# Optimization experiments

Measured on AMD Instinct MI355X. Metric: run time of the kernel, lower is better.

Reference implementation:

```python
import jax, jax.numpy as jnp
import numpy as np
import math

B, S, D, H, HD, FF, L, NS = 16, 512, 256, 8, 32, 1024, 2, 1024
THETA = 10000.0
EPS = 1e-5


def setup_inputs() -> dict:
    key = jax.random.key(0)
    ks = jax.random.split(key, 20)
    n = lambda i, shape: jax.random.normal(ks[i], shape, jnp.float32) * 0.02
    inp = {
        'values': jax.random.normal(ks[0], (B, S), jnp.float32),
        'dib': jax.random.uniform(ks[1], (B, S), jnp.float32),
        'gamma': jax.random.uniform(ks[2], (B, S), jnp.float32),
        'memory_type': jnp.ones((B, S), jnp.float32),
        'key_padding_mask': jnp.ones((B, S), dtype=bool),
        # input projection Linear(5, D)
        'in_w': n(3, (5, D)), 'in_b': jnp.zeros((D,), jnp.float32),
        # per-layer params stacked on leading L axis
        'ln1_s': jnp.ones((L, D), jnp.float32), 'ln1_b': jnp.zeros((L, D), jnp.float32),
        'qw': n(4, (L, D, D)), 'qb': jnp.zeros((L, D), jnp.float32),
        'kw': n(5, (L, D, D)), 'kb': jnp.zeros((L, D), jnp.float32),
        'vw': n(6, (L, D, D)), 'vb': jnp.zeros((L, D), jnp.float32),
        'ow': n(7, (L, D, D)), 'ob': jnp.zeros((L, D), jnp.float32),
        'ln2_s': jnp.ones((L, D), jnp.float32), 'ln2_b': jnp.zeros((L, D), jnp.float32),
        'ffw1': n(8, (L, D, FF)), 'ffb1': jnp.zeros((L, FF), jnp.float32),
        'ffw2': n(9, (L, FF, D)), 'ffb2': jnp.zeros((L, D), jnp.float32),
        'fn_s': jnp.ones((D,), jnp.float32), 'fn_b': jnp.zeros((D,), jnp.float32),
        # output head Linear(S*D, NS)
        'head_w': n(10, (S * D, NS)), 'head_b': jnp.zeros((NS,), jnp.float32),
    }
    return inp


def _layernorm(x, s, b):
    m = jnp.mean(x, axis=-1, keepdims=True)
    v = jnp.mean(jnp.square(x - m), axis=-1, keepdims=True)
    return (x - m) * jax.lax.rsqrt(v + EPS) * s + b


def _rotate_half(x):
    x1, x2 = jnp.split(x, 2, axis=-1)
    return jnp.concatenate((-x2, x1), axis=-1)


def _rope_tables():
    pos = jnp.arange(S, dtype=jnp.float32)
    inv_freq = 1.0 / (THETA ** (jnp.arange(0, HD, 2, dtype=jnp.float32) / HD))
    freqs = pos[:, None] * inv_freq[None, :]           # [S, HD/2]
    emb = jnp.concatenate((freqs, freqs), axis=-1)      # [S, HD]
    return jnp.cos(emb), jnp.sin(emb)


def _forward(values, dib, gamma, memory_type, key_padding_mask,
             in_w, in_b, ln1_s, ln1_b, qw, qb, kw, kb, vw, vb, ow, ob,
             ln2_s, ln2_b, ffw1, ffb1, ffw2, ffb2, fn_s, fn_b, head_w, head_b):
    # token features: (sign, magnitude, gamma, dib, memory_type in {-1,+1})
    sign = jnp.where(values >= 0, 1.0, -1.0)
    mt = memory_type * 2.0 - 1.0  # values in [0,1] -> signed encoding
    features = jnp.stack((sign, jnp.abs(values), gamma, dib, mt), axis=-1)  # [B,S,5]
    x = features @ in_w + in_b  # [B,S,D]

    cos, sin = _rope_tables()  # [S,HD]
    cos4 = cos[None, None]     # [1,1,S,HD]
    sin4 = sin[None, None]
    mask = key_padding_mask    # [B,S] bool
    neg = jnp.finfo(x.dtype).min
    scale = 1.0 / math.sqrt(HD)

    for l in range(L):
        h = _layernorm(x, ln1_s[l], ln1_b[l])
        q = (h @ qw[l] + qb[l]).reshape(B, S, H, HD).transpose(0, 2, 1, 3)  # [B,H,S,HD]
        k = (h @ kw[l] + kb[l]).reshape(B, S, H, HD).transpose(0, 2, 1, 3)
        v = (h @ vw[l] + vb[l]).reshape(B, S, H, HD).transpose(0, 2, 1, 3)
        q = q * cos4 + _rotate_half(q) * sin4
        k = k * cos4 + _rotate_half(k) * sin4
        scores = jnp.einsum('bhqd,bhkd->bhqk', q, k) * scale  # [B,H,S,S]
        scores = jnp.where(mask[:, None, None, :], scores, neg)
        attn = jax.nn.softmax(scores, axis=-1)
        ctx = jnp.einsum('bhqk,bhkd->bhqd', attn, v)
        ctx = ctx.transpose(0, 2, 1, 3).reshape(B, S, D)
        out = (ctx @ ow[l] + ob[l]) * mask[..., None].astype(x.dtype)
        x = x + out
        h2 = _layernorm(x, ln2_s[l], ln2_b[l])
        ff = jax.nn.gelu(h2 @ ffw1[l] + ffb1[l], approximate=False) @ ffw2[l] + ffb2[l]
        x = x + ff

    x = _layernorm(x, fn_s, fn_b)
    logits = x.reshape(B, S * D) @ head_w + head_b  # [B,NS]
    return logits


def reference(values, dib, gamma, memory_type, key_padding_mask,
              in_w, in_b, ln1_s, ln1_b, qw, qb, kw, kb, vw, vb, ow, ob,
              ln2_s, ln2_b, ffw1, ffb1, ffw2, ffb2, fn_s, fn_b, head_w, head_b):
    return _forward(values, dib, gamma, memory_type, key_padding_mask,
                    in_w, in_b, ln1_s, ln1_b, qw, qb, kw, kb, vw, vb, ow, ob,
                    ln2_s, ln2_b, ffw1, ffb1, ffw2, ffb2, fn_s, fn_b, head_w, head_b)
```

## Files before the change

kernel.cpp:

```cpp
#include <hip/hip_runtime.h>
#include <math.h>

#define BB 16
#define SS 512
#define DD 256
#define HH 8
#define HDIM 32
#define FFD 1024
#define NL 2
#define NSOUT 1024
#define SD (SS*DD)
#define ROWS (BB*SS)

#define HEAD_KC 256
#define HEAD_NCH 512

typedef __attribute__((ext_vector_type(8))) short short8;
typedef __attribute__((ext_vector_type(4))) float f32x4;

__device__ __forceinline__ unsigned short f2bf(float f) {
    union { float f; unsigned u; } c; c.f = f;
    unsigned u = c.u + 0x7fffu + ((c.u >> 16) & 1u);
    return (unsigned short)(u >> 16);
}

__device__ __forceinline__ float wave_sum(float v) {
#pragma unroll
    for (int off = 32; off > 0; off >>= 1) v += __shfl_xor(v, off);
    return v;
}
__device__ __forceinline__ float wave_max(float v) {
#pragma unroll
    for (int off = 32; off > 0; off >>= 1) v = fmaxf(v, __shfl_xor(v, off));
    return v;
}

__global__ __launch_bounds__(256) void k_rope_table(float* ct, float* st) {
    int i = blockIdx.x * 256 + threadIdx.x;
    if (i >= SS * 16) return;
    int s = i >> 4, f = i & 15;
    float invf = powf(10000.f, -(float)f / 16.f);
    float ang = (float)s * invf;
    ct[i] = cosf(ang);
    st[i] = sinf(ang);
}

__global__ __launch_bounds__(256) void k_prep_t(
    const float* __restrict__ src, unsigned short* __restrict__ dst, int K, int N) {
    __shared__ float tile[32][33];
    size_t zo = (size_t)blockIdx.z * K * N;
    int k0 = blockIdx.x * 32, n0 = blockIdx.y * 32;
    int t = threadIdx.x;
    int r = t >> 3, c4 = (t & 7) * 4;
    float4 a = *(const float4*)&src[zo + (size_t)(k0 + r) * N + n0 + c4];
    tile[r][c4 + 0] = a.x; tile[r][c4 + 1] = a.y; tile[r][c4 + 2] = a.z; tile[r][c4 + 3] = a.w;
    __syncthreads();
    unsigned o0 = f2bf(tile[c4 + 0][r]), o1 = f2bf(tile[c4 + 1][r]);
    unsigned o2 = f2bf(tile[c4 + 2][r]), o3 = f2bf(tile[c4 + 3][r]);
    uint2 ud = { o0 | (o1 << 16), o2 | (o3 << 16) };
    *(uint2*)&dst[zo + (size_t)(n0 + r) * K + k0 + c4] = ud;
}

__global__ __launch_bounds__(256) void k_input_proj(
    const float* __restrict__ values, const float* __restrict__ dib,
    const float* __restrict__ gamma, const float* __restrict__ mtyp,
    const float* __restrict__ in_w, const float* __restrict__ in_b,
    float* __restrict__ x) {
    int i = blockIdx.x * 256 + threadIdx.x;
    int row = i >> 8, d = i & 255;
    float v = values[row];
    float f0 = (v >= 0.f) ? 1.f : -1.f;
    float f1 = fabsf(v);
    float f2 = gamma[row];
    float f3 = dib[row];
    float f4 = mtyp[row] * 2.f - 1.f;
    x[i] = f0 * in_w[d] + f1 * in_w[DD + d] + f2 * in_w[2 * DD + d]
         + f3 * in_w[3 * DD + d] + f4 * in_w[4 * DD + d] + in_b[d];
}

template <bool OBF>
__global__ __launch_bounds__(256) void k_layernorm(
    const float* __restrict__ in, void* __restrict__ outp,
    const float* __restrict__ sc, const float* __restrict__ bi) {
    int row = blockIdx.x;
    int t = threadIdx.x;
    float v = in[(size_t)row * DD + t];
    __shared__ float red[8];
    int wid = t >> 6, lane = t & 63;
    float s = wave_sum(v);
    if (lane == 0) red[wid] = s;
    __syncthreads();
    float mean = (red[0] + red[1] + red[2] + red[3]) * (1.f / DD);
    float dv = v - mean;
    float s2 = wave_sum(dv * dv);
    if (lane == 0) red[4 + wid] = s2;
    __syncthreads();
    float var = (red[4] + red[5] + red[6] + red[7]) * (1.f / DD);
    float o = dv * rsqrtf(var + 1e-5f) * sc[t] + bi[t];
    if (OBF) ((unsigned short*)outp)[(size_t)row * DD + t] = f2bf(o);
    else     ((float*)outp)[(size_t)row * DD + t] = o;
}

template <int EPI, bool OBF>
__global__ __launch_bounds__(256) void k_gemm_bf16(
    const short* __restrict__ A, const short* __restrict__ Bt,
    const float* __restrict__ bias, void* __restrict__ Cout,
    int M, int N, int K, const float* __restrict__ resx, const int* __restrict__ mask) {
    __shared__ __align__(16) short As[128 * 32];
    __shared__ __align__(16) short Bs[128 * 32];
    int t = threadIdx.x;
    int lane = t & 63, wid = t >> 6;
    int wr = wid >> 1, wc = wid & 1;
    int m0 = blockIdx.x * 128, n0 = blockIdx.y * 128;
    f32x4 acc[4][4] = {};
    int srow = t >> 2, sslot = t & 3;
    for (int k0 = 0; k0 < K; k0 += 32) {
#pragma unroll
        for (int p = 0; p < 2; ++p) {
            int row = srow + p * 64;
            int sw = sslot ^ ((row >> 1) & 3);
            *(float4*)&As[row * 32 + sw * 8] =
                *(const float4*)&A[(size_t)(m0 + row) * K + k0 + sslot * 8];
            *(float4*)&Bs[row * 32 + sw * 8] =
                *(const float4*)&Bt[(size_t)(n0 + row) * K + k0 + sslot * 8];
        }
        __syncthreads();
        short8 af[4], bfr[4];
#pragma unroll
        for (int mt = 0; mt < 4; ++mt) {
            int row = wr * 64 + mt * 16 + (lane & 15);
            int sl = (lane >> 4) ^ ((row >> 1) & 3);
            af[mt] = *(const short8*)&As[row * 32 + sl * 8];
        }
#pragma unroll
        for (int nt = 0; nt < 4; ++nt) {
            int row = wc * 64 + nt * 16 + (lane & 15);
            int sl = (lane >> 4) ^ ((row >> 1) & 3);
            bfr[nt] = *(const short8*)&Bs[row * 32 + sl * 8];
        }
#pragma unroll
        for (int mt = 0; mt < 4; ++mt)
#pragma unroll
            for (int nt = 0; nt < 4; ++nt)
                acc[mt][nt] = __builtin_amdgcn_mfma_f32_16x16x32_bf16(af[mt], bfr[nt], acc[mt][nt], 0, 0, 0);
        __syncthreads();
    }
#pragma unroll
    for (int mt = 0; mt < 4; ++mt) {
#pragma unroll
        for (int i = 0; i < 4; ++i) {
            int gm = m0 + wr * 64 + mt * 16 + (lane >> 4) * 4 + i;
            float mk = 1.f;
            if (EPI == 2) mk = (mask[gm] != 0) ? 1.f : 0.f;
#pragma unroll
            for (int nt = 0; nt < 4; ++nt) {
                int gn = n0 + wc * 64 + nt * 16 + (lane & 15);
                float v = acc[mt][nt][i] + bias[gn];
                if (EPI == 1) v = 0.5f * v * (1.f + erff(v * 0.70710678118654752f));
                if (EPI == 2 || EPI == 3) v = resx[(size_t)gm * N + gn] + v * mk;
                if (OBF) ((unsigned short*)Cout)[(size_t)gm * N + gn] = f2bf(v);
                else     ((float*)Cout)[(size_t)gm * N + gn] = v;
            }
        }
    }
}

template <int EPI>
__global__ __launch_bounds__(256) void k_gemm64(
    const short* __restrict__ A, const short* __restrict__ Bt,
    const float* __restrict__ bias, float* __restrict__ Cout,
    int M, int N, int K, const float* __restrict__ resx, const int* __restrict__ mask) {
    __shared__ __align__(16) short As[64 * 32];
    __shared__ __align__(16) short Bs[128 * 32];
    int t = threadIdx.x;
    int lane = t & 63, wid = t >> 6;
    int wr = wid >> 1, wc = wid & 1;
    int m0 = blockIdx.x * 64, n0 = blockIdx.y * 128;
    f32x4 acc[2][4] = {};
    int srow = t >> 2, sslot = t & 3;
    int l15 = lane & 15, lh = lane >> 4;
    for (int k0 = 0; k0 < K; k0 += 32) {
        {
            int sw = sslot ^ ((srow >> 1) & 3);
            *(float4*)&As[srow * 32 + sw * 8] =
                *(const float4*)&A[(size_t)(m0 + srow) * K + k0 + sslot * 8];
        }
#pragma unroll
        for (int p = 0; p < 2; ++p) {
            int row = srow + p * 64;
            int sw = sslot ^ ((row >> 1) & 3);
            *(float4*)&Bs[row * 32 + sw * 8] =
                *(const float4*)&Bt[(size_t)(n0 + row) * K + k0 + sslot * 8];
        }
        __syncthreads();
        short8 af[2], bfr[4];
#pragma unroll
        for (int mt = 0; mt < 2; ++mt) {
            int row = wr * 32 + mt * 16 + l15;
            int sl = lh ^ ((row >> 1) & 3);
            af[mt] = *(const short8*)&As[row * 32 + sl * 8];
        }
#pragma unroll
        for (int nt = 0; nt < 4; ++nt) {
            int row = wc * 64 + nt * 16 + l15;
            int sl = lh ^ ((row >> 1) & 3);
            bfr[nt] = *(const short8*)&Bs[row * 32 + sl * 8];
        }
#pragma unroll
        for (int mt = 0; mt < 2; ++mt)
#pragma unroll
            for (int nt = 0; nt < 4; ++nt)
                acc[mt][nt] = __builtin_amdgcn_mfma_f32_16x16x32_bf16(af[mt], bfr[nt], acc[mt][nt], 0, 0, 0);
        __syncthreads();
    }
#pragma unroll
    for (int mt = 0; mt < 2; ++mt) {
#pragma unroll
        for (int i = 0; i < 4; ++i) {
            int gm = m0 + wr * 32 + mt * 16 + lh * 4 + i;
            float mk = 1.f;
            if (EPI == 2) mk = (mask[gm] != 0) ? 1.f : 0.f;
#pragma unroll
            for (int nt = 0; nt < 4; ++nt) {
                int gn = n0 + wc * 64 + nt * 16 + l15;
                float v = acc[mt][nt][i] + bias[gn];
                v = resx[(size_t)gm * N + gn] + v * mk;
                Cout[(size_t)gm * N + gn] = v;
            }
        }
    }
}

__global__ __launch_bounds__(256) void k_qkv(
    const short* __restrict__ A,
    const short* __restrict__ Wq, const short* __restrict__ Wk, const short* __restrict__ Wv,
    const float* __restrict__ bq, const float* __restrict__ bk, const float* __restrict__ bv,
    const float* __restrict__ ct, const float* __restrict__ st,
    unsigned short* __restrict__ q16, unsigned short* __restrict__ k16,
    unsigned short* __restrict__ vt16) {
    __shared__ __align__(16) short As[128 * 32];
    __shared__ __align__(16) short Bs[128 * 32];
    int mat = blockIdx.y >> 1;
    int n0 = (blockIdx.y & 1) * 128;
    const short* Bt = (mat == 0) ? Wq : (mat == 1) ? Wk : Wv;
    const float* bias = (mat == 0) ? bq : (mat == 1) ? bk : bv;
    int t = threadIdx.x;
    int lane = t & 63, wid = t >> 6;
    int wr = wid >> 1, wc = wid & 1;
    int m0 = blockIdx.x * 128;
    int l15 = lane & 15, lh = lane >> 4;
    f32x4 acc[4][4] = {};
    int srow = t >> 2, sslot = t & 3;
    for (int k0 = 0; k0 < DD; k0 += 32) {
#pragma unroll
        for (int p = 0; p < 2; ++p) {
            int row = srow + p * 64;
            int sw = sslot ^ ((row >> 1) & 3);
            *(float4*)&As[row * 32 + sw * 8] =
                *(const float4*)&A[(size_t)(m0 + row) * DD + k0 + sslot * 8];
            *(float4*)&Bs[row * 32 + sw * 8] =
                *(const float4*)&Bt[(size_t)(n0 + row) * DD + k0 + sslot * 8];
        }
        __syncthreads();
        short8 af[4], bfr[4];
#pragma unroll
        for (int mt = 0; mt < 4; ++mt) {
            int row = wr * 64 + mt * 16 + l15;
            int sl = lh ^ ((row >> 1) & 3);
            af[mt] = *(const short8*)&As[row * 32 + sl * 8];
        }
#pragma unroll
        for (int nt = 0; nt < 4; ++nt) {
            int row = wc * 64 + nt * 16 + l15;
            int sl = lh ^ ((row >> 1) & 3);
            bfr[nt] = *(const short8*)&Bs[row * 32 + sl * 8];
        }
#pragma unroll
        for (int mt = 0; mt < 4; ++mt)
#pragma unroll
            for (int nt = 0; nt < 4; ++nt)
                acc[mt][nt] = __builtin_amdgcn_mfma_f32_16x16x32_bf16(af[mt], bfr[nt], acc[mt][nt], 0, 0, 0);
        __syncthreads();
    }
    float bs[4];
#pragma unroll
    for (int nt = 0; nt < 4; ++nt) bs[nt] = bias[n0 + wc * 64 + nt * 16 + l15];
    if (mat < 2) {
        unsigned short* dst = (mat == 0) ? q16 : k16;
#pragma unroll
        for (int mt = 0; mt < 4; ++mt) {
#pragma unroll
            for (int i = 0; i < 4; ++i) {
                int gm = m0 + wr * 64 + mt * 16 + lh * 4 + i;
                int s = gm & (SS - 1);
                float c = ct[s * 16 + l15], sn = st[s * 16 + l15];
                float val[4];
#pragma unroll
                for (int nt = 0; nt < 4; ++nt) val[nt] = acc[mt][nt][i] + bs[nt];
#pragma unroll
                for (int nt = 0; nt < 4; ++nt) {
                    float partner = val[nt ^ 1];
                    float o = ((nt & 1) == 0) ? (val[nt] * c - partner * sn)
                                              : (val[nt] * c + partner * sn);
                    dst[(size_t)gm * DD + n0 + wc * 64 + nt * 16 + l15] = f2bf(o);
                }
            }
        }
    } else {
#pragma unroll
        for (int mt = 0; mt < 4; ++mt) {
            int gmb = m0 + wr * 64 + mt * 16 + lh * 4;
            int b = gmb >> 9, sb = gmb & (SS - 1);
#pragma unroll
            for (int nt = 0; nt < 4; ++nt) {
                int gn = n0 + wc * 64 + nt * 16 + l15;
                int h = gn >> 5, d = gn & 31;
                ushort4 u;
#pragma unroll
                for (int i = 0; i < 4; ++i)
                    (&u.x)[i] = f2bf(acc[mt][nt][i] + bs[nt]);
                *(ushort4*)&vt16[((size_t)((b * HH + h) * HDIM + d)) * SS + sb] = u;
            }
        }
    }
}

__global__ __launch_bounds__(256) void k_flash(
    const short* __restrict__ qb, const short* __restrict__ kb,
    const short* __restrict__ vt, const int* __restrict__ mask,
    unsigned short* __restrict__ ctxb) {
    __shared__ float bias_lds[SS];
    __shared__ __align__(16) short p_lds[4][32 * 72];
    __shared__ __align__(16) float r_lds[4][32];
    int t = threadIdx.x, lane = t & 63, wq = t >> 6;
    int bh = blockIdx.y;
    int b = bh >> 3, h = bh & 7;
    int q0 = blockIdx.x * 128 + wq * 32;
    bias_lds[t]       = (mask[b * SS + t]       != 0) ? 0.f : -3.0e38f;
    bias_lds[t + 256] = (mask[b * SS + t + 256] != 0) ? 0.f : -3.0e38f;
    __syncthreads();
    int l15 = lane & 15, lh = lane >> 4;
    short8 qfr[2];
    qfr[0] = *(const short8*)&qb[((size_t)(b * SS) + q0 + l15) * DD + h * HDIM + lh * 8];
    qfr[1] = *(const short8*)&qb[((size_t)(b * SS) + q0 + 16 + l15) * DD + h * HDIM + lh * 8];
    float m[2] = {-3.0e38f, -3.0e38f};
    float lsum[2] = {0.f, 0.f};
    f32x4 oacc[2][2] = {};
    const float scale = 0.17677669529663687f;
    for (int k0 = 0; k0 < SS; k0 += 64) {
        f32x4 sT[4][2];
#pragma unroll
        for (int kt = 0; kt < 4; ++kt) {
            short8 kf = *(const short8*)&kb[((size_t)(b * SS) + k0 + kt * 16 + l15) * DD + h * HDIM + lh * 8];
#pragma unroll
            for (int qf = 0; qf < 2; ++qf) {
                f32x4 z = {0.f, 0.f, 0.f, 0.f};
                sT[kt][qf] = __builtin_amdgcn_mfma_f32_16x16x32_bf16(kf, qfr[qf], z, 0, 0, 0);
            }
        }
        float p[2][16];
        float r[2];
#pragma unroll
        for (int qf = 0; qf < 2; ++qf) {
            float pmax = -3.0e38f;
#pragma unroll
            for (int kt = 0; kt < 4; ++kt)
#pragma unroll
                for (int i = 0; i < 4; ++i) {
                    float s = sT[kt][qf][i] * scale + bias_lds[k0 + kt * 16 + lh * 4 + i];
                    p[qf][kt * 4 + i] = s;
                    pmax = fmaxf(pmax, s);
                }
            pmax = fmaxf(pmax, __shfl_xor(pmax, 16));
            pmax = fmaxf(pmax, __shfl_xor(pmax, 32));
            float mn = fmaxf(m[qf], pmax);
            r[qf] = expf(m[qf] - mn);
            m[qf] = mn;
            float cs = 0.f;
#pragma unroll
            for (int j = 0; j < 16; ++j) {
                float e = expf(p[qf][j] - mn);
                p[qf][j] = e;
                cs += e;
            }
            cs += __shfl_xor(cs, 16);
            cs += __shfl_xor(cs, 32);
            lsum[qf] = lsum[qf] * r[qf] + cs;
        }
#pragma unroll
        for (int qf = 0; qf < 2; ++qf) {
            int qq = qf * 16 + l15;
#pragma unroll
            for (int kt = 0; kt < 4; ++kt) {
                unsigned u0 = (unsigned)f2bf(p[qf][kt * 4 + 0]) | ((unsigned)f2bf(p[qf][kt * 4 + 1]) << 16);
                unsigned u1 = (unsigned)f2bf(p[qf][kt * 4 + 2]) | ((unsigned)f2bf(p[qf][kt * 4 + 3]) << 16);
                uint2 u = { u0, u1 };
                *(uint2*)&p_lds[wq][qq * 72 + kt * 16 + lh * 4] = u;
            }
        }
        if (lane < 16) { r_lds[wq][l15] = r[0]; r_lds[wq][16 + l15] = r[1]; }
        __syncthreads();
#pragma unroll
        for (int mf = 0; mf < 2; ++mf) {
            float4 rv = *(const float4*)&r_lds[wq][mf * 16 + lh * 4];
#pragma unroll
            for (int df = 0; df < 2; ++df) {
                oacc[mf][df][0] *= rv.x; oacc[mf][df][1] *= rv.y;
                oacc[mf][df][2] *= rv.z; oacc[mf][df][3] *= rv.w;
            }
        }
#pragma unroll
        for (int ks = 0; ks < 2; ++ks) {
            short8 pa0 = *(const short8*)&p_lds[wq][(l15) * 72 + ks * 32 + lh * 8];
            short8 pa1 = *(const short8*)&p_lds[wq][(16 + l15) * 72 + ks * 32 + lh * 8];
#pragma unroll
            for (int df = 0; df < 2; ++df) {
                short8 vf = *(const short8*)&vt[((size_t)bh * HDIM + df * 16 + l15) * SS + k0 + ks * 32 + lh * 8];
                oacc[0][df] = __builtin_amdgcn_mfma_f32_16x16x32_bf16(pa0, vf, oacc[0][df], 0, 0, 0);
                oacc[1][df] = __builtin_amdgcn_mfma_f32_16x16x32_bf16(pa1, vf, oacc[1][df], 0, 0, 0);
            }
        }
        __syncthreads();
    }
    if (lane < 16) { r_lds[wq][l15] = 1.f / lsum[0]; r_lds[wq][16 + l15] = 1.f / lsum[1]; }
    __syncthreads();
#pragma unroll
    for (int mf = 0; mf < 2; ++mf) {
        float4 lv = *(const float4*)&r_lds[wq][mf * 16 + lh * 4];
        const float li[4] = { lv.x, lv.y, lv.z, lv.w };
#pragma unroll
        for (int df = 0; df < 2; ++df)
#pragma unroll
            for (int i = 0; i < 4; ++i) {
                int gq = q0 + mf * 16 + lh * 4 + i;
                int gd = df * 16 + l15;
                ctxb[((size_t)(b * SS) + gq) * DD + h * HDIM + gd] = f2bf(oacc[mf][df][i] * li[i]);
            }
    }
}

__global__ __launch_bounds__(256) void k_head_part(
    const float* __restrict__ x, const float* __restrict__ W,
    float* __restrict__ part) {
    __shared__ float xs[16 * HEAD_KC];
    int c = blockIdx.x;
    int k0 = c * HEAD_KC;
    int t = threadIdx.x;
#pragma unroll
    for (int b = 0; b < 16; ++b)
        xs[b * HEAD_KC + t] = x[(size_t)b * SD + k0 + t];
    __syncthreads();
    int n4 = t * 4;
    float acc[16][4] = {};
#pragma unroll 4
    for (int k = 0; k < HEAD_KC; ++k) {
        float4 w = *(const float4*)&W[(size_t)(k0 + k) * NSOUT + n4];
#pragma unroll
        for (int b = 0; b < 16; ++b) {
            float xv = xs[b * HEAD_KC + k];
            acc[b][0] += xv * w.x; acc[b][1] += xv * w.y;
            acc[b][2] += xv * w.z; acc[b][3] += xv * w.w;
        }
    }
#pragma unroll
    for (int b = 0; b < 16; ++b) {
        float4 o = {acc[b][0], acc[b][1], acc[b][2], acc[b][3]};
        *(float4*)&part[((size_t)c * 16 + b) * NSOUT + n4] = o;
    }
}

__global__ __launch_bounds__(256) void k_head_reduce(
    const float* __restrict__ part, const float* __restrict__ hb,
    float* __restrict__ out) {
    int i = (blockIdx.x * 256 + threadIdx.x) * 4;
    float4 s = {0.f, 0.f, 0.f, 0.f};
#pragma unroll 8
    for (int c = 0; c < HEAD_NCH; ++c) {
        float4 p = *(const float4*)&part[(size_t)c * (16 * NSOUT) + i];
        s.x += p.x; s.y += p.y; s.z += p.z; s.w += p.w;
    }
    int n = i & (NSOUT - 1);
    float4 b4 = *(const float4*)&hb[n];
    float4 o = {s.x + b4.x, s.y + b4.y, s.z + b4.z, s.w + b4.w};
    *(float4*)&out[i] = o;
}

extern "C" void kernel_launch(void* const* d_in, const int* in_sizes, int n_in,
                              void* d_out, int out_size, void* d_ws, size_t ws_size,
                              hipStream_t stream) {
    const float* values = (const float*)d_in[0];
    const float* dib    = (const float*)d_in[1];
    const float* gamma  = (const float*)d_in[2];
    const float* mtyp   = (const float*)d_in[3];
    const int*   mask   = (const int*)d_in[4];
    const float* in_w   = (const float*)d_in[5];
    const float* in_b   = (const float*)d_in[6];
    const float* ln1_s  = (const float*)d_in[7];
    const float* ln1_b  = (const float*)d_in[8];
    const float* p_qw   = (const float*)d_in[9];
    const float* p_qb   = (const float*)d_in[10];
    const float* p_kw   = (const float*)d_in[11];
    const float* p_kb   = (const float*)d_in[12];
    const float* p_vw   = (const float*)d_in[13];
    const float* p_vb   = (const float*)d_in[14];
    const float* p_ow   = (const float*)d_in[15];
    const float* p_ob   = (const float*)d_in[16];
    const float* ln2_s  = (const float*)d_in[17];
    const float* ln2_b  = (const float*)d_in[18];
    const float* p_f1w  = (const float*)d_in[19];
    const float* p_f1b  = (const float*)d_in[20];
    const float* p_f2w  = (const float*)d_in[21];
    const float* p_f2b  = (const float*)d_in[22];
    const float* fn_s   = (const float*)d_in[23];
    const float* fn_b   = (const float*)d_in[24];
    const float* head_w = (const float*)d_in[25];
    const float* head_b = (const float*)d_in[26];
    float* out = (float*)d_out;

    const size_t MB = 1u << 20;
    char* w = (char*)d_ws;
    float* x    = (float*)(w + 0 * MB);
    float* qf   = (float*)(w + 8 * MB);
    unsigned short* h16  = (unsigned short*)(w + 32 * MB);
    unsigned short* q16  = (unsigned short*)(w + 36 * MB);
    unsigned short* k16  = (unsigned short*)(w + 40 * MB);
    unsigned short* vt16 = (unsigned short*)(w + 44 * MB);
    unsigned short* cx16 = (unsigned short*)(w + 48 * MB);
    unsigned short* f116 = (unsigned short*)(w + 52 * MB);
    unsigned short* wq16 = (unsigned short*)(w + 68 * MB);
    unsigned short* wk16 = (unsigned short*)(w + 68 * MB + 256 * 1024);
    unsigned short* wv16 = (unsigned short*)(w + 68 * MB + 512 * 1024);
    unsigned short* wo16 = (unsigned short*)(w + 68 * MB + 768 * 1024);
    unsigned short* wf116 = (unsigned short*)(w + 69 * MB);
    unsigned short* wf216 = (unsigned short*)(w + 70 * MB);
    float* ct   = (float*)(w + 71 * MB);
    float* st   = (float*)(w + 71 * MB + 64 * 1024);
    float* sc   = (float*)(w + 72 * MB);

    k_rope_table<<<32, 256, 0, stream>>>(ct, st);
    k_prep_t<<<dim3(8, 8, NL), 256, 0, stream>>>(p_qw, wq16, DD, DD);
    k_prep_t<<<dim3(8, 8, NL), 256, 0, stream>>>(p_kw, wk16, DD, DD);
    k_prep_t<<<dim3(8, 8, NL), 256, 0, stream>>>(p_vw, wv16, DD, DD);
    k_prep_t<<<dim3(8, 8, NL), 256, 0, stream>>>(p_ow, wo16, DD, DD);
    k_prep_t<<<dim3(8, 32, NL), 256, 0, stream>>>(p_f1w, wf116, DD, FFD);
    k_prep_t<<<dim3(32, 8, NL), 256, 0, stream>>>(p_f2w, wf216, FFD, DD);
    k_input_proj<<<8192, 256, 0, stream>>>(values, dib, gamma, mtyp, in_w, in_b, x);

    for (int l = 0; l < NL; ++l) {
        k_layernorm<true><<<ROWS, 256, 0, stream>>>(x, h16, ln1_s + l * DD, ln1_b + l * DD);
        k_qkv<<<dim3(64, 6), 256, 0, stream>>>((const short*)h16,
            (const short*)(wq16 + l * 65536), (const short*)(wk16 + l * 65536),
            (const short*)(wv16 + l * 65536),
            p_qb + l * DD, p_kb + l * DD, p_vb + l * DD, ct, st, q16, k16, vt16);
        k_flash<<<dim3(4, BB * HH), 256, 0, stream>>>((const short*)q16, (const short*)k16,
            (const short*)vt16, mask, cx16);
        k_gemm64<2><<<dim3(128, 2), 256, 0, stream>>>((const short*)cx16,
            (const short*)(wo16 + l * 65536), p_ob + l * DD, x, ROWS, DD, DD, x, mask);
        k_layernorm<true><<<ROWS, 256, 0, stream>>>(x, h16, ln2_s + l * DD, ln2_b + l * DD);
        k_gemm_bf16<1, true><<<dim3(64, 8), 256, 0, stream>>>((const short*)h16,
            (const short*)(wf116 + l * 262144), p_f1b + l * FFD, f116,
            ROWS, FFD, DD, nullptr, nullptr);
        k_gemm64<3><<<dim3(128, 2), 256, 0, stream>>>((const short*)f116,
            (const short*)(wf216 + l * 262144), p_f2b + l * DD, x, ROWS, DD, FFD, x, nullptr);
    }

    k_layernorm<false><<<ROWS, 256, 0, stream>>>(x, qf, fn_s, fn_b);
    k_head_part<<<HEAD_NCH, 256, 0, stream>>>(qf, head_w, sc);
    k_head_reduce<<<16, 256, 0, stream>>>(sc, head_b, out);
}
```

Baseline: 371.1 us.

## Merge prep kernels, wave-per-row layernorm, retile GEMMs, fold attention scale into Q

Merges the weight-transpose and RoPE-table kernels into a single launch, cutting launch overhead. Layernorm now gives each row to one wavefront with float4 loads and a one-pass sum and sum-of-squares, which removes block barriers. The k_gemm64 k-step grows to 64 with an 8-way swizzle, and QKV moves to 64-row tiles to launch more blocks. The softmax scale is folded into Q, attention uses fast __expf, and the head GEMM uses nontemporal weight loads with deeper unrolling. The one-pass variance and fast exp carry small numerical risk.

```diff
diff --git a/kernel.cpp b/kernel.cpp
--- a/kernel.cpp
+++ b/kernel.cpp
@@ -24,41 +24,52 @@
     return (unsigned short)(u >> 16);
 }
 
-__device__ __forceinline__ float wave_sum(float v) {
-#pragma unroll
-    for (int off = 32; off > 0; off >>= 1) v += __shfl_xor(v, off);
-    return v;
-}
-__device__ __forceinline__ float wave_max(float v) {
-#pragma unroll
-    for (int off = 32; off > 0; off >>= 1) v = fmaxf(v, __shfl_xor(v, off));
-    return v;
-}
-
-__global__ __launch_bounds__(256) void k_rope_table(float* ct, float* st) {
-    int i = blockIdx.x * 256 + threadIdx.x;
-    if (i >= SS * 16) return;
-    int s = i >> 4, f = i & 15;
-    float invf = powf(10000.f, -(float)f / 16.f);
-    float ang = (float)s * invf;
-    ct[i] = cosf(ang);
-    st[i] = sinf(ang);
-}
-
-__global__ __launch_bounds__(256) void k_prep_t(
-    const float* __restrict__ src, unsigned short* __restrict__ dst, int K, int N) {
+__global__ __launch_bounds__(256) void k_prep_all(
+    const float* __restrict__ p_qw, const float* __restrict__ p_kw,
+    const float* __restrict__ p_vw, const float* __restrict__ p_ow,
+    const float* __restrict__ p_f1w, const float* __restrict__ p_f2w,
+    unsigned short* __restrict__ wq, unsigned short* __restrict__ wk,
+    unsigned short* __restrict__ wv, unsigned short* __restrict__ wo,
+    unsigned short* __restrict__ wf1, unsigned short* __restrict__ wf2,
+    float* __restrict__ ct, float* __restrict__ st) {
+    int bid = blockIdx.x;
+    int t = threadIdx.x;
+    if (bid >= 1536) {
+        int i = (bid - 1536) * 256 + t;
+        if (i < SS * 16) {
+            int s = i >> 4, f = i & 15;
+            float invf = powf(10000.f, -(float)f / 16.f);
+            float ang = (float)s * invf;
+            ct[i] = cosf(ang);
+            st[i] = sinf(ang);
+        }
+        return;
+    }
+    const float* src; unsigned short* dst;
+    int K, N, kx, nx, l;
+    if (bid < 512) {
+        int grp = bid >> 7, r = bid & 127; l = r >> 6; int tl = r & 63;
+        kx = tl >> 3; nx = tl & 7; K = DD; N = DD;
+        src = grp == 0 ? p_qw : grp == 1 ? p_kw : grp == 2 ? p_vw : p_ow;
+        dst = grp == 0 ? wq : grp == 1 ? wk : grp == 2 ? wv : wo;
+    } else if (bid < 1024) {
+        int r = bid - 512; l = r >> 8; int tl = r & 255;
+        kx = tl >> 5; nx = tl & 31; K = DD; N = FFD; src = p_f1w; dst = wf1;
+    } else {
+        int r = bid - 1024; l = r >> 8; int tl = r & 255;
+        kx = tl >> 3; nx = tl & 7; K = FFD; N = DD; src = p_f2w; dst = wf2;
+    }
     __shared__ float tile[32][33];
-    size_t zo = (size_t)blockIdx.z * K * N;
-    int k0 = blockIdx.x * 32, n0 = blockIdx.y * 32;
-    int t = threadIdx.x;
-    int r = t >> 3, c4 = (t & 7) * 4;
-    float4 a = *(const float4*)&src[zo + (size_t)(k0 + r) * N + n0 + c4];
-    tile[r][c4 + 0] = a.x; tile[r][c4 + 1] = a.y; tile[r][c4 + 2] = a.z; tile[r][c4 + 3] = a.w;
+    size_t zo = (size_t)l * K * N;
+    int k0 = kx * 32, n0 = nx * 32;
+    int r_ = t >> 3, c4 = (t & 7) * 4;
+    float4 a = *(const float4*)&src[zo + (size_t)(k0 + r_) * N + n0 + c4];
+    tile[r_][c4 + 0] = a.x; tile[r_][c4 + 1] = a.y; tile[r_][c4 + 2] = a.z; tile[r_][c4 + 3] = a.w;
     __syncthreads();
-    unsigned o0 = f2bf(tile[c4 + 0][r]), o1 = f2bf(tile[c4 + 1][r]);
-    unsigned o2 = f2bf(tile[c4 + 2][r]), o3 = f2bf(tile[c4 + 3][r]);
+    unsigned o0 = f2bf(tile[c4 + 0][r_]), o1 = f2bf(tile[c4 + 1][r_]);
+    unsigned o2 = f2bf(tile[c4 + 2][r_]), o3 = f2bf(tile[c4 + 3][r_]);
     uint2 ud = { o0 | (o1 << 16), o2 | (o3 << 16) };
-    *(uint2*)&dst[zo + (size_t)(n0 + r) * K + k0 + c4] = ud;
+    *(uint2*)&dst[zo + (size_t)(n0 + r_) * K + k0 + c4] = ud;
 }
 
 __global__ __launch_bounds__(256) void k_input_proj(
@@ -79,33 +90,41 @@
 }
 
 template <bool OBF>
-__global__ __launch_bounds__(256) void k_layernorm(
+__global__ __launch_bounds__(256) void k_layernorm_w(
     const float* __restrict__ in, void* __restrict__ outp,
     const float* __restrict__ sc, const float* __restrict__ bi) {
-    int row = blockIdx.x;
-    int t = threadIdx.x;
-    float v = in[(size_t)row * DD + t];
-    __shared__ float red[8];
-    int wid = t >> 6, lane = t & 63;
-    float s = wave_sum(v);
-    if (lane == 0) red[wid] = s;
-    __syncthreads();
-    float mean = (red[0] + red[1] + red[2] + red[3]) * (1.f / DD);
-    float dv = v - mean;
-    float s2 = wave_sum(dv * dv);
-    if (lane == 0) red[4 + wid] = s2;
-    __syncthreads();
-    float var = (red[4] + red[5] + red[6] + red[7]) * (1.f / DD);
-    float o = dv * rsqrtf(var + 1e-5f) * sc[t] + bi[t];
-    if (OBF) ((unsigned short*)outp)[(size_t)row * DD + t] = f2bf(o);
-    else     ((float*)outp)[(size_t)row * DD + t] = o;
-}
-
-template <int EPI, bool OBF>
-__global__ __launch_bounds__(256) void k_gemm_bf16(
+    int t = threadIdx.x, lane = t & 63, w = t >> 6;
+    int row = blockIdx.x * 4 + w;
+    float4 v = *(const float4*)&in[(size_t)row * DD + lane * 4];
+    float s1 = v.x + v.y + v.z + v.w;
+    float s2 = v.x * v.x + v.y * v.y + v.z * v.z + v.w * v.w;
+#pragma unroll
+    for (int off = 32; off > 0; off >>= 1) {
+        s1 += __shfl_xor(s1, off);
+        s2 += __shfl_xor(s2, off);
+    }
+    float mean = s1 * (1.f / DD);
+    float var = s2 * (1.f / DD) - mean * mean;
+    float rstd = rsqrtf(var + 1e-5f);
+    float4 sv = *(const float4*)&sc[lane * 4];
+    float4 bv = *(const float4*)&bi[lane * 4];
+    float o0 = (v.x - mean) * rstd * sv.x + bv.x;
+    float o1 = (v.y - mean) * rstd * sv.y + bv.y;
+    float o2 = (v.z - mean) * rstd * sv.z + bv.z;
+    float o3 = (v.w - mean) * rstd * sv.w + bv.w;
+    if (OBF) {
+        ushort4 u = { f2bf(o0), f2bf(o1), f2bf(o2), f2bf(o3) };
+        *(ushort4*)&((unsigned short*)outp)[(size_t)row * DD + lane * 4] = u;
+    } else {
+        float4 o = { o0, o1, o2, o3 };
+        *(float4*)&((float*)outp)[(size_t)row * DD + lane * 4] = o;
+    }
+}
+
+__global__ __launch_bounds__(256) void k_gemm_ff1(
     const short* __restrict__ A, const short* __restrict__ Bt,
-    const float* __restrict__ bias, void* __restrict__ Cout,
-    int M, int N, int K, const float* __restrict__ resx, const int* __restrict__ mask) {
+    const float* __restrict__ bias, unsigned short* __restrict__ Cout,
+    int M, int N, int K) {
     __shared__ __align__(16) short As[128 * 32];
     __shared__ __align__(16) short Bs[128 * 32];
     int t = threadIdx.x;
@@ -150,16 +169,12 @@
 #pragma unroll
         for (int i = 0; i < 4; ++i) {
             int gm = m0 + wr * 64 + mt * 16 + (lane >> 4) * 4 + i;
-            float mk = 1.f;
-            if (EPI == 2) mk = (mask[gm] != 0) ? 1.f : 0.f;
 #pragma unroll
             for (int nt = 0; nt < 4; ++nt) {
                 int gn = n0 + wc * 64 + nt * 16 + (lane & 15);
                 float v = acc[mt][nt][i] + bias[gn];
-                if (EPI == 1) v = 0.5f * v * (1.f + erff(v * 0.70710678118654752f));
-                if (EPI == 2 || EPI == 3) v = resx[(size_t)gm * N + gn] + v * mk;
-                if (OBF) ((unsigned short*)Cout)[(size_t)gm * N + gn] = f2bf(v);
-                else     ((float*)Cout)[(size_t)gm * N + gn] = v;
+                v = 0.5f * v * (1.f + erff(v * 0.70710678118654752f));
+                Cout[(size_t)gm * N + gn] = f2bf(v);
             }
         }
     }
@@ -170,47 +185,53 @@
     const short* __restrict__ A, const short* __restrict__ Bt,
     const float* __restrict__ bias, float* __restrict__ Cout,
     int M, int N, int K, const float* __restrict__ resx, const int* __restrict__ mask) {
-    __shared__ __align__(16) short As[64 * 32];
-    __shared__ __align__(16) short Bs[128 * 32];
+    __shared__ __align__(16) short As[64 * 64];
+    __shared__ __align__(16) short Bs[128 * 64];
     int t = threadIdx.x;
     int lane = t & 63, wid = t >> 6;
     int wr = wid >> 1, wc = wid & 1;
     int m0 = blockIdx.x * 64, n0 = blockIdx.y * 128;
+    int l15 = lane & 15, lh = lane >> 4;
     f32x4 acc[2][4] = {};
-    int srow = t >> 2, sslot = t & 3;
-    int l15 = lane & 15, lh = lane >> 4;
-    for (int k0 = 0; k0 < K; k0 += 32) {
-        {
-            int sw = sslot ^ ((srow >> 1) & 3);
-            *(float4*)&As[srow * 32 + sw * 8] =
-                *(const float4*)&A[(size_t)(m0 + srow) * K + k0 + sslot * 8];
-        }
+    for (int k0 = 0; k0 < K; k0 += 64) {
 #pragma unroll
         for (int p = 0; p < 2; ++p) {
-            int row = srow + p * 64;
-            int sw = sslot ^ ((row >> 1) & 3);
-            *(float4*)&Bs[row * 32 + sw * 8] =
-                *(const float4*)&Bt[(size_t)(n0 + row) * K + k0 + sslot * 8];
-        }
-        __syncthreads();
-        short8 af[2], bfr[4];
-#pragma unroll
-        for (int mt = 0; mt < 2; ++mt) {
-            int row = wr * 32 + mt * 16 + l15;
-            int sl = lh ^ ((row >> 1) & 3);
-            af[mt] = *(const short8*)&As[row * 32 + sl * 8];
-        }
-#pragma unroll
-        for (int nt = 0; nt < 4; ++nt) {
-            int row = wc * 64 + nt * 16 + l15;
-            int sl = lh ^ ((row >> 1) & 3);
-            bfr[nt] = *(const short8*)&Bs[row * 32 + sl * 8];
-        }
-#pragma unroll
-        for (int mt = 0; mt < 2; ++mt)
-#pragma unroll
-            for (int nt = 0; nt < 4; ++nt)
-                acc[mt][nt] = __builtin_amdgcn_mfma_f32_16x16x32_bf16(af[mt], bfr[nt], acc[mt][nt], 0, 0, 0);
+            int idx = t + p * 256;
+            int row = idx >> 3, sl = idx & 7;
+            int sw = sl ^ (row & 7);
+            *(float4*)&As[row * 64 + sw * 8] =
+                *(const float4*)&A[(size_t)(m0 + row) * K + k0 + sl * 8];
+        }
+#pragma unroll
+        for (int p = 0; p < 4; ++p) {
+            int idx = t + p * 256;
+            int row = idx >> 3, sl = idx & 7;
+            int sw = sl ^ (row & 7);
+            *(float4*)&Bs[row * 64 + sw * 8] =
+                *(const float4*)&Bt[(size_t)(n0 + row) * K + k0 + sl * 8];
+        }
+        __syncthreads();
+#pragma unroll
+        for (int kk = 0; kk < 2; ++kk) {
+            short8 af[2], bfr[4];
+#pragma unroll
+            for (int mt = 0; mt < 2; ++mt) {
+                int row = wr * 32 + mt * 16 + l15;
+                int sl = (kk * 4 + lh) ^ (row & 7);
+                af[mt] = *(const short8*)&As[row * 64 + sl * 8];
+            }
+#pragma unroll
+            for (int nt = 0; nt < 4; ++nt) {
+                int row = wc * 64 + nt * 16 + l15;
+                int sl = (kk * 4 + lh) ^ (row & 7);
+                bfr[nt] = *(const short8*)&Bs[row * 64 + sl * 8];
+            }
+#pragma unroll
+            for (int mt = 0; mt < 2; ++mt)
+#pragma unroll
+                for (int nt = 0; nt < 4; ++nt)
+                    acc[mt][nt] = __builtin_amdgcn_mfma_f32_16x16x32_bf16(af[mt], bfr[nt], acc[mt][nt], 0, 0, 0);
+        }
         __syncthreads();
     }
 #pragma unroll
@@ -231,14 +252,14 @@
     }
 }
 
-__global__ __launch_bounds__(256) void k_qkv(
+__global__ __launch_bounds__(256) void k_qkv64(
     const short* __restrict__ A,
     const short* __restrict__ Wq, const short* __restrict__ Wk, const short* __restrict__ Wv,
     const float* __restrict__ bq, const float* __restrict__ bk, const float* __restrict__ bv,
     const float* __restrict__ ct, const float* __restrict__ st,
     unsigned short* __restrict__ q16, unsigned short* __restrict__ k16,
     unsigned short* __restrict__ vt16) {
-    __shared__ __align__(16) short As[128 * 32];
+    __shared__ __align__(16) short As[64 * 32];
     __shared__ __align__(16) short Bs[128 * 32];
     int mat = blockIdx.y >> 1;
     int n0 = (blockIdx.y & 1) * 128;
@@ -247,25 +268,28 @@
     int t = threadIdx.x;
     int lane = t & 63, wid = t >> 6;
     int wr = wid >> 1, wc = wid & 1;
-    int m0 = blockIdx.x * 128;
+    int m0 = blockIdx.x * 64;
     int l15 = lane & 15, lh = lane >> 4;
-    f32x4 acc[4][4] = {};
+    f32x4 acc[2][4] = {};
     int srow = t >> 2, sslot = t & 3;
     for (int k0 = 0; k0 < DD; k0 += 32) {
+        {
+            int sw = sslot ^ ((srow >> 1) & 3);
+            *(float4*)&As[srow * 32 + sw * 8] =
+                *(const float4*)&A[(size_t)(m0 + srow) * DD + k0 + sslot * 8];
+        }
 #pragma unroll
         for (int p = 0; p < 2; ++p) {
             int row = srow + p * 64;
             int sw = sslot ^ ((row >> 1) & 3);
-            *(float4*)&As[row * 32 + sw * 8] =
-                *(const float4*)&A[(size_t)(m0 + row) * DD + k0 + sslot * 8];
             *(float4*)&Bs[row * 32 + sw * 8] =
                 *(const float4*)&Bt[(size_t)(n0 + row) * DD + k0 + sslot * 8];
         }
         __syncthreads();
-        short8 af[4], bfr[4];
-#pragma unroll
-        for (int mt = 0; mt < 4; ++mt) {
-            int row = wr * 64 + mt * 16 + l15;
+        short8 af[2], bfr[4];
+#pragma unroll
+        for (int mt = 0; mt < 2; ++mt) {
+            int row = wr * 32 + mt * 16 + l15;
             int sl = lh ^ ((row >> 1) & 3);
             af[mt] = *(const short8*)&As[row * 32 + sl * 8];
         }
@@ -276,7 +300,7 @@
             bfr[nt] = *(const short8*)&Bs[row * 32 + sl * 8];
         }
 #pragma unroll
-        for (int mt = 0; mt < 4; ++mt)
+        for (int mt = 0; mt < 2; ++mt)
 #pragma unroll
             for (int nt = 0; nt < 4; ++nt)
                 acc[mt][nt] = __builtin_amdgcn_mfma_f32_16x16x32_bf16(af[mt], bfr[nt], acc[mt][nt], 0, 0, 0);
@@ -287,16 +311,17 @@
     for (int nt = 0; nt < 4; ++nt) bs[nt] = bias[n0 + wc * 64 + nt * 16 + l15];
     if (mat < 2) {
         unsigned short* dst = (mat == 0) ? q16 : k16;
-#pragma unroll
-        for (int mt = 0; mt < 4; ++mt) {
+        const float qscale = (mat == 0) ? 0.17677669529663687f : 1.f;
+#pragma unroll
+        for (int mt = 0; mt < 2; ++mt) {
 #pragma unroll
             for (int i = 0; i < 4; ++i) {
-                int gm = m0 + wr * 64 + mt * 16 + lh * 4 + i;
+                int gm = m0 + wr * 32 + mt * 16 + lh * 4 + i;
                 int s = gm & (SS - 1);
                 float c = ct[s * 16 + l15], sn = st[s * 16 + l15];
                 float val[4];
 #pragma unroll
-                for (int nt = 0; nt < 4; ++nt) val[nt] = acc[mt][nt][i] + bs[nt];
+                for (int nt = 0; nt < 4; ++nt) val[nt] = (acc[mt][nt][i] + bs[nt]) * qscale;
 #pragma unroll
                 for (int nt = 0; nt < 4; ++nt) {
                     float partner = val[nt ^ 1];
@@ -308,8 +333,8 @@
         }
     } else {
 #pragma unroll
-        for (int mt = 0; mt < 4; ++mt) {
-            int gmb = m0 + wr * 64 + mt * 16 + lh * 4;
+        for (int mt = 0; mt < 2; ++mt) {
+            int gmb = m0 + wr * 32 + mt * 16 + lh * 4;
             int b = gmb >> 9, sb = gmb & (SS - 1);
 #pragma unroll
             for (int nt = 0; nt < 4; ++nt) {
@@ -346,7 +371,6 @@
     float m[2] = {-3.0e38f, -3.0e38f};
     float lsum[2] = {0.f, 0.f};
     f32x4 oacc[2][2] = {};
-    const float scale = 0.17677669529663687f;
     for (int k0 = 0; k0 < SS; k0 += 64) {
         f32x4 sT[4][2];
 #pragma unroll
@@ -367,19 +391,19 @@
             for (int kt = 0; kt < 4; ++kt)
 #pragma unroll
                 for (int i = 0; i < 4; ++i) {
-                    float s = sT[kt][qf][i] * scale + bias_lds[k0 + kt * 16 + lh * 4 + i];
+                    float s = sT[kt][qf][i] + bias_lds[k0 + kt * 16 + lh * 4 + i];
                     p[qf][kt * 4 + i] = s;
                     pmax = fmaxf(pmax, s);
                 }
             pmax = fmaxf(pmax, __shfl_xor(pmax, 16));
             pmax = fmaxf(pmax, __shfl_xor(pmax, 32));
             float mn = fmaxf(m[qf], pmax);
-            r[qf] = expf(m[qf] - mn);
+            r[qf] = __expf(m[qf] - mn);
             m[qf] = mn;
             float cs = 0.f;
 #pragma unroll
             for (int j = 0; j < 16; ++j) {
-                float e = expf(p[qf][j] - mn);
+                float e = __expf(p[qf][j] - mn);
                 p[qf][j] = e;
                 cs += e;
             }
@@ -452,14 +476,14 @@
     __syncthreads();
     int n4 = t * 4;
     float acc[16][4] = {};
-#pragma unroll 4
+#pragma unroll 8
     for (int k = 0; k < HEAD_KC; ++k) {
-        float4 w = *(const float4*)&W[(size_t)(k0 + k) * NSOUT + n4];
+        f32x4 w = __builtin_nontemporal_load((const f32x4*)&W[(size_t)(k0 + k) * NSOUT + n4]);
 #pragma unroll
         for (int b = 0; b < 16; ++b) {
             float xv = xs[b * HEAD_KC + k];
-            acc[b][0] += xv * w.x; acc[b][1] += xv * w.y;
-            acc[b][2] += xv * w.z; acc[b][3] += xv * w.w;
+            acc[b][0] += xv * w[0]; acc[b][1] += xv * w[1];
+            acc[b][2] += xv * w[2]; acc[b][3] += xv * w[3];
         }
     }
 #pragma unroll
@@ -537,18 +561,13 @@
     float* st   = (float*)(w + 71 * MB + 64 * 1024);
     float* sc   = (float*)(w + 72 * MB);
 
-    k_rope_table<<<32, 256, 0, stream>>>(ct, st);
-    k_prep_t<<<dim3(8, 8, NL), 256, 0, stream>>>(p_qw, wq16, DD, DD);
-    k_prep_t<<<dim3(8, 8, NL), 256, 0, stream>>>(p_kw, wk16, DD, DD);
-    k_prep_t<<<dim3(8, 8, NL), 256, 0, stream>>>(p_vw, wv16, DD, DD);
-    k_prep_t<<<dim3(8, 8, NL), 256, 0, stream>>>(p_ow, wo16, DD, DD);
-    k_prep_t<<<dim3(8, 32, NL), 256, 0, stream>>>(p_f1w, wf116, DD, FFD);
-    k_prep_t<<<dim3(32, 8, NL), 256, 0, stream>>>(p_f2w, wf216, FFD, DD);
+    k_prep_all<<<1568, 256, 0, stream>>>(p_qw, p_kw, p_vw, p_ow, p_f1w, p_f2w,
+                                         wq16, wk16, wv16, wo16, wf116, wf216, ct, st);
     k_input_proj<<<8192, 256, 0, stream>>>(values, dib, gamma, mtyp, in_w, in_b, x);
 
     for (int l = 0; l < NL; ++l) {
-        k_layernorm<true><<<ROWS, 256, 0, stream>>>(x, h16, ln1_s + l * DD, ln1_b + l * DD);
-        k_qkv<<<dim3(64, 6), 256, 0, stream>>>((const short*)h16,
+        k_layernorm_w<true><<<2048, 256, 0, stream>>>(x, h16, ln1_s + l * DD, ln1_b + l * DD);
+        k_qkv64<<<dim3(128, 6), 256, 0, stream>>>((const short*)h16,
             (const short*)(wq16 + l * 65536), (const short*)(wk16 + l * 65536),
             (const short*)(wv16 + l * 65536),
             p_qb + l * DD, p_kb + l * DD, p_vb + l * DD, ct, st, q16, k16, vt16);
@@ -556,15 +575,14 @@
             (const short*)vt16, mask, cx16);
         k_gemm64<2><<<dim3(128, 2), 256, 0, stream>>>((const short*)cx16,
             (const short*)(wo16 + l * 65536), p_ob + l * DD, x, ROWS, DD, DD, x, mask);
-        k_layernorm<true><<<ROWS, 256, 0, stream>>>(x, h16, ln2_s + l * DD, ln2_b + l * DD);
-        k_gemm_bf16<1, true><<<dim3(64, 8), 256, 0, stream>>>((const short*)h16,
-            (const short*)(wf116 + l * 262144), p_f1b + l * FFD, f116,
-            ROWS, FFD, DD, nullptr, nullptr);
+        k_layernorm_w<true><<<2048, 256, 0, stream>>>(x, h16, ln2_s + l * DD, ln2_b + l * DD);
+        k_gemm_ff1<<<dim3(64, 8), 256, 0, stream>>>((const short*)h16,
+            (const short*)(wf116 + l * 262144), p_f1b + l * FFD, f116, ROWS, FFD, DD);
         k_gemm64<3><<<dim3(128, 2), 256, 0, stream>>>((const short*)f116,
             (const short*)(wf216 + l * 262144), p_f2b + l * DD, x, ROWS, DD, FFD, x, nullptr);
     }
 
-    k_layernorm<false><<<ROWS, 256, 0, stream>>>(x, qf, fn_s, fn_b);
+    k_layernorm_w<false><<<2048, 256, 0, stream>>>(x, qf, fn_s, fn_b);
     k_head_part<<<HEAD_NCH, 256, 0, stream>>>(qf, head_w, sc);
     k_head_reduce<<<16, 256, 0, stream>>>(sc, head_b, out);
 }
```

Result: no change. 365.3 us (-1.6%).
